# Optimization experiments

Measured on AMD Instinct MI355X. Metric: run time of the kernel, lower is better.

Reference implementation:

```python
import jax, jax.numpy as jnp
import numpy as np

DIM_IN = 1024
DIM_OUT = 1024
NUM_HEADS = 16
HEAD_DIM = DIM_OUT // NUM_HEADS


def setup_inputs() -> dict:
    key = jax.random.key(0)
    k1, k2, k3, k4 = jax.random.split(key, 4)
    X = jax.random.normal(k1, (4, 2048, DIM_IN), dtype=jnp.float32)
    W_qkv = jax.random.normal(k2, (DIM_IN, 3 * DIM_OUT), dtype=jnp.float32) * (DIM_IN ** -0.5)
    W_out = jax.random.normal(k3, (DIM_OUT, DIM_OUT), dtype=jnp.float32) * (DIM_OUT ** -0.5)
    b_out = jax.random.normal(k4, (DIM_OUT,), dtype=jnp.float32) * 0.01
    return {"X": X, "W_qkv": W_qkv, "W_out": W_out, "b_out": b_out}


def reference(X, W_qkv, W_out, b_out):
    B, S, _ = X.shape
    qkv = X @ W_qkv  # [B, S, 3*dim_out]
    qkv = qkv.reshape(B, S, 3, NUM_HEADS, HEAD_DIM).transpose(2, 0, 3, 1, 4)
    q, k, v = qkv[0], qkv[1], qkv[2]  # each [B, H, S, hd]
    scores = jnp.einsum('bhqd,bhkd->bhqk', q, k)  # [B, H, S, S]
    causal = jnp.triu(jnp.ones((S, S), dtype=bool), k=1)
    scores = jnp.where(causal, -jnp.inf, scores)
    attn = jax.nn.softmax(scores * (HEAD_DIM ** -0.5), axis=-1)
    ctx = jnp.einsum('bhqk,bhkd->bhqd', attn, v)  # [B, H, S, hd]
    ctx = ctx.transpose(0, 2, 1, 3).reshape(B, S, DIM_OUT)
    return ctx @ W_out + b_out
```

## Files before the change

### kernel.cpp

```cpp
#include <hip/hip_runtime.h>
#include <hip/hip_bf16.h>

typedef __bf16 bf16_t;
typedef __bf16 bf16x8 __attribute__((ext_vector_type(8)));
typedef __bf16 bf16x4 __attribute__((ext_vector_type(4)));
typedef float f32x4 __attribute__((ext_vector_type(4)));
typedef float f32x16 __attribute__((ext_vector_type(16)));
typedef unsigned int u32x4 __attribute__((ext_vector_type(4)));

#define AS1(p) ((const __attribute__((address_space(1))) void*)(p))
#define AS3(p) ((__attribute__((address_space(3))) void*)(p))

#define QSCALE 0.1803368801111204f

__global__ __launch_bounds__(256) void prep_kernel(
    const float* __restrict__ X, bf16_t* __restrict__ Xb,
    const float* __restrict__ Wqkv, bf16_t* __restrict__ Wqkvt,
    const float* __restrict__ Wout, bf16_t* __restrict__ Woutt) {
  __shared__ float tile[32][33];
  int bid = blockIdx.x;
  if (bid < 8192) {
    int i = (bid * 256 + threadIdx.x) * 4;
    float4 v = *(const float4*)(X + i);
    bf16x4 o;
    o[0] = (bf16_t)v.x; o[1] = (bf16_t)v.y; o[2] = (bf16_t)v.z; o[3] = (bf16_t)v.w;
    *(bf16x4*)(Xb + i) = o;
    return;
  }
  bid -= 8192;
  const float* W; bf16_t* Wt; int N, bx, by;
  if (bid < 3072) { W = Wqkv; Wt = Wqkvt; N = 3072; bx = bid % 96; by = bid / 96; }
  else { bid -= 3072; W = Wout; Wt = Woutt; N = 1024; bx = bid & 31; by = bid >> 5; }
  const int K = 1024;
  int tx = threadIdx.x & 31, ty = threadIdx.x >> 5;
  int n0 = bx * 32, k0 = by * 32;
  for (int r = ty; r < 32; r += 8)
    tile[r][tx] = W[(size_t)(k0 + r) * N + n0 + tx];
  __syncthreads();
  for (int r = ty; r < 32; r += 8)
    Wt[(size_t)(n0 + r) * K + k0 + tx] = (bf16_t)tile[tx][r];
}

__global__ __launch_bounds__(256) void gemm_qkv_kernel(
    const bf16_t* __restrict__ A, const bf16_t* __restrict__ Bt,
    bf16_t* __restrict__ Qb, bf16_t* __restrict__ Kb, bf16_t* __restrict__ Vt) {
  __shared__ __align__(16) bf16_t As[128 * 64];
  __shared__ __align__(16) bf16_t Bs[128 * 64];
  const int tid = threadIdx.x;
  const int lane = tid & 63, wave = tid >> 6;
  const int quad = lane >> 4, l15 = lane & 15;
  const int wr = wave >> 1, wc = wave & 1;
  const int bid = blockIdx.x;
  const int mt_ = (bid & 7) * 8 + ((bid >> 3) & 7);
  const int nt_ = bid >> 6;
  const int m0 = mt_ * 128, n0 = nt_ * 128;
  f32x4 acc[4][4];
  const f32x4 vzero = {0.f, 0.f, 0.f, 0.f};
#pragma unroll
  for (int i = 0; i < 4; i++)
#pragma unroll
    for (int j = 0; j < 4; j++) acc[i][j] = vzero;

  for (int kb = 0; kb < 1024; kb += 64) {
    __syncthreads();
#pragma unroll
    for (int i = 0; i < 4; i++) {
      int slot = i * 256 + tid;
      int row = slot >> 3, ch = slot & 7;
      int gch = ch ^ (row & 7);
      __builtin_amdgcn_global_load_lds(AS1(A + (size_t)(m0 + row) * 1024 + kb + gch * 8),
                                       AS3(As + slot * 8), 16, 0, 0);
    }
#pragma unroll
    for (int i = 0; i < 4; i++) {
      int slot = i * 256 + tid;
      int row = slot >> 3, ch = slot & 7;
      int gch = ch ^ (row & 7);
      __builtin_amdgcn_global_load_lds(AS1(Bt + (size_t)(n0 + row) * 1024 + kb + gch * 8),
                                       AS3(Bs + slot * 8), 16, 0, 0);
    }
    __builtin_amdgcn_s_waitcnt(0);
    __syncthreads();
#pragma unroll
    for (int ks = 0; ks < 2; ks++) {
      bf16x8 af[4], bfr[4];
#pragma unroll
      for (int t = 0; t < 4; t++) {
        int ra = wr * 64 + t * 16 + l15;
        af[t]  = *(const bf16x8*)(As + ra * 64 + ((ks * 4 + quad) ^ (ra & 7)) * 8);
        int rb = wc * 64 + t * 16 + l15;
        bfr[t] = *(const bf16x8*)(Bs + rb * 64 + ((ks * 4 + quad) ^ (rb & 7)) * 8);
      }
#pragma unroll
      for (int mt = 0; mt < 4; mt++)
#pragma unroll
        for (int nt = 0; nt < 4; nt++)
          acc[mt][nt] = __builtin_amdgcn_mfma_f32_16x16x32_bf16(af[mt], bfr[nt], acc[mt][nt], 0, 0, 0);
    }
  }
#pragma unroll
  for (int nt = 0; nt < 4; nt++) {
    int gn = n0 + wc * 64 + nt * 16 + l15;
    int which = gn >> 10;
    int rem = gn & 1023;
    int hh = rem >> 6, dd = rem & 63;
    if (which == 2) {
#pragma unroll
      for (int mt = 0; mt < 4; mt++) {
        int gm0 = m0 + wr * 64 + mt * 16 + quad * 4;
        int b = gm0 >> 11, s = gm0 & 2047;
        bf16x4 o;
#pragma unroll
        for (int r = 0; r < 4; r++) o[r] = (bf16_t)acc[mt][nt][r];
        *(bf16x4*)(Vt + ((size_t)((b << 4) + hh) * 64 + dd) * 2048 + s) = o;
      }
    } else {
      bf16_t* dst = (which == 0) ? Qb : Kb;
      float scl = (which == 0) ? QSCALE : 1.0f;
#pragma unroll
      for (int mt = 0; mt < 4; mt++) {
#pragma unroll
        for (int r = 0; r < 4; r++) {
          int gm = m0 + wr * 64 + mt * 16 + quad * 4 + r;
          int b = gm >> 11, s = gm & 2047;
          dst[((size_t)((b << 4) + hh) * 2048 + s) * 64 + dd] = (bf16_t)(acc[mt][nt][r] * scl);
        }
      }
    }
  }
}

__device__ inline unsigned pack_bf16x2(float a, float b) {
  unsigned short lo = __builtin_bit_cast(unsigned short, (bf16_t)a);
  unsigned short hi = __builtin_bit_cast(unsigned short, (bf16_t)b);
  return (unsigned)lo | ((unsigned)hi << 16);
}

__global__ __launch_bounds__(256, 4) void attn_kernel(
    const bf16_t* __restrict__ Qg_, const bf16_t* __restrict__ Kg_,
    const bf16_t* __restrict__ Vtg_, bf16_t* __restrict__ ctx) {
  __shared__ __align__(16) bf16_t Ksm[2][64 * 64];
  __shared__ __align__(16) bf16_t Vsm[2][64 * 64];
  __shared__ float Lsh[128];
  const int tid = threadIdx.x;
  const int lane = tid & 63, w = tid >> 6;
  const int l31 = lane & 31, hl = lane >> 5;
  const int krow = (l31 & 0x13) | ((l31 & 4) << 1) | ((l31 & 8) >> 1);

  const int bh = blockIdx.x & 63;
  const int g = blockIdx.x >> 6;
  const int gr = g >> 2, gc = g & 3;
  const int qb = (gr == 0) ? (15 - gc) : (gr == 1) ? (8 + gc) : (gr == 2) ? (7 - gc) : gc;
  const int b = bh >> 4, h = bh & 15;
  const size_t base = (size_t)bh * 2048 * 64;
  const bf16_t* Qg = Qg_ + base;
  const bf16_t* Kg = Kg_ + base;
  const bf16_t* Vtg = Vtg_ + base;

  int kadr[4];
#pragma unroll
  for (int kk = 0; kk < 4; kk++)
    kadr[kk] = (krow * 8 + ((kk * 2 + hl) ^ (krow & 7))) * 8;
  int vadr[2];
#pragma unroll
  for (int nv = 0; nv < 2; nv++) {
    const int dr = nv * 32 + l31;
    vadr[nv] = (dr * 8 + (hl ^ (dr & 7))) * 8;
  }

  auto stage_kv = [&](int bb, int jn) {
#pragma unroll
    for (int i = 0; i < 2; i++) {
      int slot = i * 256 + tid;
      int row = slot >> 3, c = (slot & 7) ^ (row & 7);
      __builtin_amdgcn_global_load_lds(AS1(Kg + ((size_t)jn * 64 + row) * 64 + c * 8),
                                       AS3(&Ksm[bb][0] + slot * 8), 16, 0, 0);
    }
#pragma unroll
    for (int i = 0; i < 2; i++) {
      int slot = i * 256 + tid;
      int d = slot >> 3, c = (slot & 7) ^ (d & 7);
      __builtin_amdgcn_global_load_lds(AS1(Vtg + (size_t)d * 2048 + jn * 64 + c * 8),
                                       AS3(&Vsm[bb][0] + slot * 8), 16, 0, 0);
    }
  };

  f32x16 zc;
#pragma unroll
  for (int e = 0; e < 16; e++) zc[e] = 0.f;

  const int J = 2 * (qb + 1);
  const int qrel = qb * 128 + w * 32;
  const int qg = qrel + l31;

  bf16x8 aq[4];
#pragma unroll
  for (int kk = 0; kk < 4; kk++)
    aq[kk] = *(const bf16x8*)(Qg + (size_t)qg * 64 + kk * 16 + hl * 8);

  f32x16 Oacc[2];
#pragma unroll
  for (int e = 0; e < 16; e++) { Oacc[0][e] = 0.f; Oacc[1][e] = 0.f; }
  float Lpart = 0.f;

  int cur = 0;
  stage_kv(0, 0);

  for (int j = 0; j < J; j++) {
    asm volatile("s_waitcnt vmcnt(0)" ::: "memory");
    __syncthreads();
    if (j + 1 < J) stage_kv(cur ^ 1, j + 1);

    const bf16_t* Kb = &Ksm[cur][0];
    const bf16_t* Vb = &Vsm[cur][0];
    const int k0 = j * 64;

    auto nt_body = [&](int nt, bool masked) {
      __builtin_amdgcn_s_setprio(1);
      bf16x8 a0 = *(const bf16x8*)(Kb + nt * 2048 + kadr[0]);
      bf16x8 a1 = *(const bf16x8*)(Kb + nt * 2048 + kadr[1]);
      f32x16 sa = __builtin_amdgcn_mfma_f32_32x32x16_bf16(a0, aq[0], zc, 0, 0, 0);
      f32x16 sb = __builtin_amdgcn_mfma_f32_32x32x16_bf16(a1, aq[1], zc, 0, 0, 0);
      bf16x8 a2 = *(const bf16x8*)(Kb + nt * 2048 + kadr[2]);
      bf16x8 a3 = *(const bf16x8*)(Kb + nt * 2048 + kadr[3]);
      sa = __builtin_amdgcn_mfma_f32_32x32x16_bf16(a2, aq[2], sa, 0, 0, 0);
      sb = __builtin_amdgcn_mfma_f32_32x32x16_bf16(a3, aq[3], sb, 0, 0, 0);
      __builtin_amdgcn_s_setprio(0);

      float p[16];
#pragma unroll
      for (int r = 0; r < 16; r++) {
        const int koff = hl * 8 + (r & 7) + 16 * (r >> 3);
        const float x = sa[r] + sb[r];
        p[r] = (masked && (koff > l31)) ? 0.f : __builtin_exp2f(x);
      }

      {
        float a0s = p[0] + p[1], a1s = p[2] + p[3], a2s = p[4] + p[5], a3s = p[6] + p[7];
        float a4s = p[8] + p[9], a5s = p[10] + p[11], a6s = p[12] + p[13], a7s = p[14] + p[15];
        Lpart += ((a0s + a1s) + (a2s + a3s)) + ((a4s + a5s) + (a6s + a7s));
      }

      u32x4 w0, w1;
      w0[0] = pack_bf16x2(p[0], p[1]);   w0[1] = pack_bf16x2(p[2], p[3]);
      w0[2] = pack_bf16x2(p[4], p[5]);   w0[3] = pack_bf16x2(p[6], p[7]);
      w1[0] = pack_bf16x2(p[8], p[9]);   w1[1] = pack_bf16x2(p[10], p[11]);
      w1[2] = pack_bf16x2(p[12], p[13]); w1[3] = pack_bf16x2(p[14], p[15]);
      bf16x8 pa0 = __builtin_bit_cast(bf16x8, w0);
      bf16x8 pa1 = __builtin_bit_cast(bf16x8, w1);

      __builtin_amdgcn_s_setprio(1);
#pragma unroll
      for (int nv = 0; nv < 2; nv++) {
        bf16x8 bv0 = *(const bf16x8*)(Vb + (vadr[nv] ^ ((nt * 4 + 0) * 8)));
        Oacc[nv] = __builtin_amdgcn_mfma_f32_32x32x16_bf16(pa0, bv0, Oacc[nv], 0, 0, 0);
        bf16x8 bv1 = *(const bf16x8*)(Vb + (vadr[nv] ^ ((nt * 4 + 2) * 8)));
        Oacc[nv] = __builtin_amdgcn_mfma_f32_32x32x16_bf16(pa1, bv1, Oacc[nv], 0, 0, 0);
      }
      __builtin_amdgcn_s_setprio(0);
    };

#pragma unroll
    for (int nt = 0; nt < 2; nt++) {
      const int kk0 = k0 + nt * 32;
      if (kk0 <= qrel) nt_body(nt, kk0 == qrel);
    }
    cur ^= 1;
  }

  float Lf = Lpart + __shfl_xor(Lpart, 32, 64);
  if (hl == 0) Lsh[w * 32 + l31] = Lf;
  asm volatile("s_waitcnt lgkmcnt(0)" ::: "memory");
#pragma unroll
  for (int r = 0; r < 16; r++) {
    const int crow = (r & 3) + 8 * (r >> 2) + 4 * hl;
    const float rl = __builtin_amdgcn_rcpf(Lsh[w * 32 + crow]);
    const int qrow = qb * 128 + w * 32 + crow;
#pragma unroll
    for (int nv = 0; nv < 2; nv++)
      ctx[((size_t)b * 2048 + qrow) * 1024 + h * 64 + nv * 32 + l31] =
          (bf16_t)(Oacc[nv][r] * rl);
  }
}

__global__ __launch_bounds__(256) void gemm_out_kernel(
    const bf16_t* __restrict__ A, const bf16_t* __restrict__ Bt,
    const float* __restrict__ bias, float* __restrict__ out) {
  __shared__ __align__(16) bf16_t As[128 * 64];
  __shared__ __align__(16) bf16_t Bs[128 * 64];
  const int tid = threadIdx.x;
  const int lane = tid & 63, wave = tid >> 6;
  const int quad = lane >> 4, l15 = lane & 15;
  const int wr = wave >> 1, wc = wave & 1;
  const int bid = blockIdx.x;
  const int mt_ = (bid & 7) * 8 + ((bid >> 3) & 7);
  const int nt_ = bid >> 6;
  const int m0 = mt_ * 128, n0 = nt_ * 128;
  f32x4 acc[4][4];
  const f32x4 vzero = {0.f, 0.f, 0.f, 0.f};
#pragma unroll
  for (int i = 0; i < 4; i++)
#pragma unroll
    for (int j = 0; j < 4; j++) acc[i][j] = vzero;

  for (int kb = 0; kb < 1024; kb += 64) {
    __syncthreads();
#pragma unroll
    for (int i = 0; i < 4; i++) {
      int slot = i * 256 + tid;
      int row = slot >> 3, ch = slot & 7;
      int gch = ch ^ (row & 7);
      __builtin_amdgcn_global_load_lds(AS1(A + (size_t)(m0 + row) * 1024 + kb + gch * 8),
                                       AS3(As + slot * 8), 16, 0, 0);
    }
#pragma unroll
    for (int i = 0; i < 4; i++) {
      int slot = i * 256 + tid;
      int row = slot >> 3, ch = slot & 7;
      int gch = ch ^ (row & 7);
      __builtin_amdgcn_global_load_lds(AS1(Bt + (size_t)(n0 + row) * 1024 + kb + gch * 8),
                                       AS3(Bs + slot * 8), 16, 0, 0);
    }
    __builtin_amdgcn_s_waitcnt(0);
    __syncthreads();
#pragma unroll
    for (int ks = 0; ks < 2; ks++) {
      bf16x8 af[4], bfr[4];
#pragma unroll
      for (int t = 0; t < 4; t++) {
        int ra = wr * 64 + t * 16 + l15;
        af[t]  = *(const bf16x8*)(As + ra * 64 + ((ks * 4 + quad) ^ (ra & 7)) * 8);
        int rb = wc * 64 + t * 16 + l15;
        bfr[t] = *(const bf16x8*)(Bs + rb * 64 + ((ks * 4 + quad) ^ (rb & 7)) * 8);
      }
#pragma unroll
      for (int mt = 0; mt < 4; mt++)
#pragma unroll
        for (int nt = 0; nt < 4; nt++)
          acc[mt][nt] = __builtin_amdgcn_mfma_f32_16x16x32_bf16(af[mt], bfr[nt], acc[mt][nt], 0, 0, 0);
    }
  }
#pragma unroll
  for (int nt = 0; nt < 4; nt++) {
    int gn = n0 + wc * 64 + nt * 16 + l15;
    float bv = bias[gn];
#pragma unroll
    for (int mt = 0; mt < 4; mt++) {
#pragma unroll
      for (int r = 0; r < 4; r++) {
        int gm = m0 + wr * 64 + mt * 16 + quad * 4 + r;
        out[(size_t)gm * 1024 + gn] = acc[mt][nt][r] + bv;
      }
    }
  }
}

extern "C" void kernel_launch(void* const* d_in, const int* in_sizes, int n_in,
                              void* d_out, int out_size, void* d_ws, size_t ws_size,
                              hipStream_t stream) {
  (void)in_sizes; (void)n_in; (void)out_size; (void)ws_size;
  const float* X     = (const float*)d_in[0];
  const float* W_qkv = (const float*)d_in[1];
  const float* W_out = (const float*)d_in[2];
  const float* b_out = (const float*)d_in[3];
  float* out = (float*)d_out;

  char* ws = (char*)d_ws;
  bf16_t* Xb    = (bf16_t*)(ws);
  bf16_t* Wqkvt = (bf16_t*)(ws + 16777216);
  bf16_t* Woutt = (bf16_t*)(ws + 23068672);
  bf16_t* Qb    = (bf16_t*)(ws + 25165824);
  bf16_t* Kb    = (bf16_t*)(ws + 41943040);
  bf16_t* Vt    = (bf16_t*)(ws + 58720256);
  bf16_t* ctx   = (bf16_t*)(ws + 75497472);

  prep_kernel<<<12288, 256, 0, stream>>>(X, Xb, W_qkv, Wqkvt, W_out, Woutt);
  gemm_qkv_kernel<<<1536, 256, 0, stream>>>(Xb, Wqkvt, Qb, Kb, Vt);
  attn_kernel<<<dim3(1024), 256, 0, stream>>>(Qb, Kb, Vt, ctx);
  gemm_out_kernel<<<512, 256, 0, stream>>>(ctx, Woutt, b_out, out);
}
```

Baseline: 246.9 us.

## Balance causal attention work by pairing query blocks and splitting KV across blocks

Each attention workgroup now runs a fixed 17 KV-tile iterations. It pairs a short query block p with part of the long block 15-p, and the long block's KV range is split between two workgroups. Partial unnormalized outputs and row sums are written to fp32 workspace buffers and merged by a new attn_norm_kernel. This targets load imbalance from the causal triangle, where some blocks did 32 tiles and others only 2. In exchange it adds a kernel launch plus extra global traffic for the fp32 partials, and it reuses workspace regions such as the Xb area.

```diff
diff --git a/kernel.cpp b/kernel.cpp
--- a/kernel.cpp
+++ b/kernel.cpp
@@ -138,7 +138,9 @@
 
 __global__ __launch_bounds__(256, 4) void attn_kernel(
     const bf16_t* __restrict__ Qg_, const bf16_t* __restrict__ Kg_,
-    const bf16_t* __restrict__ Vtg_, bf16_t* __restrict__ ctx) {
+    const bf16_t* __restrict__ Vtg_, bf16_t* __restrict__ ctx,
+    float* __restrict__ PA, float* __restrict__ PB,
+    float* __restrict__ LA, float* __restrict__ LB) {
   __shared__ __align__(16) bf16_t Ksm[2][64 * 64];
   __shared__ __align__(16) bf16_t Vsm[2][64 * 64];
   __shared__ float Lsh[128];
@@ -148,9 +150,11 @@
   const int krow = (l31 & 0x13) | ((l31 & 4) << 1) | ((l31 & 8) >> 1);
 
   const int bh = blockIdx.x & 63;
-  const int g = blockIdx.x >> 6;
-  const int gr = g >> 2, gc = g & 3;
-  const int qb = (gr == 0) ? (15 - gc) : (gr == 1) ? (8 + gc) : (gr == 2) ? (7 - gc) : gc;
+  const int pp = (blockIdx.x >> 6) & 7;
+  const int ab = blockIdx.x >> 9;
+  const int p = pp, Pq = 15 - pp;
+  const int Jp = 2 * (p + 1);
+  const int mA = 15 - 2 * p;
   const int b = bh >> 4, h = bh & 15;
   const size_t base = (size_t)bh * 2048 * 64;
   const bf16_t* Qg = Qg_ + base;
@@ -189,14 +193,19 @@
 #pragma unroll
   for (int e = 0; e < 16; e++) zc[e] = 0.f;
 
-  const int J = 2 * (qb + 1);
-  const int qrel = qb * 128 + w * 32;
-  const int qg = qrel + l31;
-
+  const int tix = bh * 8 + pp;
+  float* Pp = (ab ? PB : PA) + (size_t)tix * (128 * 64);
+  float* Lp = (ab ? LB : LA) + tix * 128;
+
+  int qrel = (ab ? Pq : p) * 128 + w * 32;
   bf16x8 aq[4];
-#pragma unroll
-  for (int kk = 0; kk < 4; kk++)
-    aq[kk] = *(const bf16x8*)(Qg + (size_t)qg * 64 + kk * 16 + hl * 8);
+  auto load_aq = [&](int qb_) {
+    const int qgl = qb_ * 128 + w * 32 + l31;
+#pragma unroll
+    for (int kk = 0; kk < 4; kk++)
+      aq[kk] = *(const bf16x8*)(Qg + (size_t)qgl * 64 + kk * 16 + hl * 8);
+  };
+  load_aq(ab ? Pq : p);
 
   f32x16 Oacc[2];
 #pragma unroll
@@ -204,15 +213,19 @@
   float Lpart = 0.f;
 
   int cur = 0;
-  stage_kv(0, 0);
-
-  for (int j = 0; j < J; j++) {
+  stage_kv(0, ab ? mA : 0);
+
+  for (int i = 0; i < 17; ++i) {
     asm volatile("s_waitcnt vmcnt(0)" ::: "memory");
     __syncthreads();
-    if (j + 1 < J) stage_kv(cur ^ 1, j + 1);
-
+    if (i + 1 < 17) {
+      const int ni = i + 1;
+      const int nj = ab ? (mA + ni) : (ni < Jp ? ni : ni - Jp);
+      stage_kv(cur ^ 1, nj);
+    }
     const bf16_t* Kb = &Ksm[cur][0];
     const bf16_t* Vb = &Vsm[cur][0];
+    const int j = ab ? (mA + i) : (i < Jp ? i : i - Jp);
     const int k0 = j * 64;
 
     auto nt_body = [&](int nt, bool masked) {
@@ -227,25 +240,25 @@
       sb = __builtin_amdgcn_mfma_f32_32x32x16_bf16(a3, aq[3], sb, 0, 0, 0);
       __builtin_amdgcn_s_setprio(0);
 
-      float p[16];
+      float p16[16];
 #pragma unroll
       for (int r = 0; r < 16; r++) {
         const int koff = hl * 8 + (r & 7) + 16 * (r >> 3);
         const float x = sa[r] + sb[r];
-        p[r] = (masked && (koff > l31)) ? 0.f : __builtin_exp2f(x);
-      }
-
+        p16[r] = (masked && (koff > l31)) ? 0.f : __builtin_exp2f(x);
+      }
       {
-        float a0s = p[0] + p[1], a1s = p[2] + p[3], a2s = p[4] + p[5], a3s = p[6] + p[7];
-        float a4s = p[8] + p[9], a5s = p[10] + p[11], a6s = p[12] + p[13], a7s = p[14] + p[15];
+        float a0s = p16[0] + p16[1], a1s = p16[2] + p16[3];
+        float a2s = p16[4] + p16[5], a3s = p16[6] + p16[7];
+        float a4s = p16[8] + p16[9], a5s = p16[10] + p16[11];
+        float a6s = p16[12] + p16[13], a7s = p16[14] + p16[15];
         Lpart += ((a0s + a1s) + (a2s + a3s)) + ((a4s + a5s) + (a6s + a7s));
       }
-
       u32x4 w0, w1;
-      w0[0] = pack_bf16x2(p[0], p[1]);   w0[1] = pack_bf16x2(p[2], p[3]);
-      w0[2] = pack_bf16x2(p[4], p[5]);   w0[3] = pack_bf16x2(p[6], p[7]);
-      w1[0] = pack_bf16x2(p[8], p[9]);   w1[1] = pack_bf16x2(p[10], p[11]);
-      w1[2] = pack_bf16x2(p[12], p[13]); w1[3] = pack_bf16x2(p[14], p[15]);
+      w0[0] = pack_bf16x2(p16[0], p16[1]);   w0[1] = pack_bf16x2(p16[2], p16[3]);
+      w0[2] = pack_bf16x2(p16[4], p16[5]);   w0[3] = pack_bf16x2(p16[6], p16[7]);
+      w1[0] = pack_bf16x2(p16[8], p16[9]);   w1[1] = pack_bf16x2(p16[10], p16[11]);
+      w1[2] = pack_bf16x2(p16[12], p16[13]); w1[3] = pack_bf16x2(p16[14], p16[15]);
       bf16x8 pa0 = __builtin_bit_cast(bf16x8, w0);
       bf16x8 pa1 = __builtin_bit_cast(bf16x8, w1);
 
@@ -260,26 +273,76 @@
       __builtin_amdgcn_s_setprio(0);
     };
 
-#pragma unroll
-    for (int nt = 0; nt < 2; nt++) {
-      const int kk0 = k0 + nt * 32;
-      if (kk0 <= qrel) nt_body(nt, kk0 == qrel);
+    if (!ab && i >= Jp) {
+      nt_body(0, false);
+      nt_body(1, false);
+    } else {
+#pragma unroll
+      for (int nt = 0; nt < 2; nt++) {
+        const int kk0 = k0 + nt * 32;
+        if (kk0 <= qrel) nt_body(nt, kk0 == qrel);
+      }
+    }
+
+    if (!ab && i == Jp - 1) {
+      float Lf = Lpart + __shfl_xor(Lpart, 32, 64);
+      if (hl == 0) Lsh[w * 32 + l31] = Lf;
+      asm volatile("s_waitcnt lgkmcnt(0)" ::: "memory");
+#pragma unroll
+      for (int r = 0; r < 16; r++) {
+        const int crow = (r & 3) + 8 * (r >> 2) + 4 * hl;
+        const float rl = __builtin_amdgcn_rcpf(Lsh[w * 32 + crow]);
+        const int qrow = p * 128 + w * 32 + crow;
+#pragma unroll
+        for (int nv = 0; nv < 2; nv++)
+          ctx[((size_t)b * 2048 + qrow) * 1024 + h * 64 + nv * 32 + l31] =
+              (bf16_t)(Oacc[nv][r] * rl);
+      }
+#pragma unroll
+      for (int e = 0; e < 16; e++) { Oacc[0][e] = 0.f; Oacc[1][e] = 0.f; }
+      Lpart = 0.f;
+      load_aq(Pq);
+      qrel = Pq * 128 + w * 32;
     }
     cur ^= 1;
   }
 
   float Lf = Lpart + __shfl_xor(Lpart, 32, 64);
-  if (hl == 0) Lsh[w * 32 + l31] = Lf;
-  asm volatile("s_waitcnt lgkmcnt(0)" ::: "memory");
+  if (hl == 0) Lp[w * 32 + l31] = Lf;
 #pragma unroll
   for (int r = 0; r < 16; r++) {
     const int crow = (r & 3) + 8 * (r >> 2) + 4 * hl;
-    const float rl = __builtin_amdgcn_rcpf(Lsh[w * 32 + crow]);
-    const int qrow = qb * 128 + w * 32 + crow;
+    const int row = w * 32 + crow;
 #pragma unroll
     for (int nv = 0; nv < 2; nv++)
-      ctx[((size_t)b * 2048 + qrow) * 1024 + h * 64 + nv * 32 + l31] =
-          (bf16_t)(Oacc[nv][r] * rl);
+      Pp[row * 64 + nv * 32 + l31] = Oacc[nv][r];
+  }
+}
+
+__global__ __launch_bounds__(256) void attn_norm_kernel(
+    const float* __restrict__ PA, const float* __restrict__ PB,
+    const float* __restrict__ LA, const float* __restrict__ LB,
+    bf16_t* __restrict__ ctx) {
+  const int t = blockIdx.x;
+  const int bh = t >> 3, pp = t & 7;
+  const int Pq = 15 - pp;
+  const int b = bh >> 4, h = bh & 15;
+  const float4* pa = (const float4*)(PA + (size_t)t * 8192);
+  const float4* pb = (const float4*)(PB + (size_t)t * 8192);
+  const float* la = LA + t * 128;
+  const float* lb = LB + t * 128;
+#pragma unroll
+  for (int k = 0; k < 8; k++) {
+    const int v = threadIdx.x + k * 256;
+    const int row = v >> 4, dd = (v & 15) * 4;
+    float4 a = pa[v], c = pb[v];
+    const float rl = __builtin_amdgcn_rcpf(la[row] + lb[row]);
+    bf16x4 o;
+    o[0] = (bf16_t)((a.x + c.x) * rl);
+    o[1] = (bf16_t)((a.y + c.y) * rl);
+    o[2] = (bf16_t)((a.z + c.z) * rl);
+    o[3] = (bf16_t)((a.w + c.w) * rl);
+    *(bf16x4*)(ctx + ((size_t)b * 2048 + Pq * 128 + row) * 1024 + h * 64 + dd) = o;
   }
 }
 
@@ -373,9 +436,14 @@
   bf16_t* Kb    = (bf16_t*)(ws + 41943040);
   bf16_t* Vt    = (bf16_t*)(ws + 58720256);
   bf16_t* ctx   = (bf16_t*)(ws + 75497472);
+  float* PA = (float*)(ws);
+  float* LA = (float*)(ws + 16777216);
+  float* LB = (float*)(ws + 17039360);
+  float* PB = (float*)(ws + 92274688);
 
   prep_kernel<<<12288, 256, 0, stream>>>(X, Xb, W_qkv, Wqkvt, W_out, Woutt);
   gemm_qkv_kernel<<<1536, 256, 0, stream>>>(Xb, Wqkvt, Qb, Kb, Vt);
-  attn_kernel<<<dim3(1024), 256, 0, stream>>>(Qb, Kb, Vt, ctx);
+  attn_kernel<<<dim3(1024), 256, 0, stream>>>(Qb, Kb, Vt, ctx, PA, PB, LA, LB);
+  attn_norm_kernel<<<512, 256, 0, stream>>>(PA, PB, LA, LB, ctx);
   gemm_out_kernel<<<512, 256, 0, stream>>>(ctx, Woutt, b_out, out);
 }
```

Measured after the change: 622.2 us. +152.1%, slower.
